# Optimization experiments

Measured on AMD Instinct MI355X. Metric: run time of the kernel, lower is better.

Reference implementation:

```python
import jax, jax.numpy as jnp
import numpy as np

N = 10000; E = 320000; NFEAT = 500; NHID = 256; C = 16; K = 64
GAMMA = 4; ALPHA = 0.1; BETA = 1.0; EPS = 0.1; LAMDA = 0.5; W1 = 0.5

def _init(key, shape, scale=0.05):
    return jax.random.normal(key, shape, dtype=jnp.float32) * scale

def setup_inputs():
    key = jax.random.key(0)
    ks = jax.random.split(key, 24)
    return {
        "x": jax.random.normal(ks[0], (N, NFEAT), dtype=jnp.float32),
        "edge_index": jax.random.randint(ks[1], (2, E), 0, N),
        "edge_weight": jax.random.uniform(ks[2], (E,), dtype=jnp.float32),
        "adj_weight": jax.random.uniform(ks[3], (E,), dtype=jnp.float32),
        "connect": jax.random.uniform(ks[4], (N, N), dtype=jnp.float32),
        "confidence_in": jax.random.uniform(ks[5], (2, E), dtype=jnp.float32),
        "lin1_w": _init(ks[6], (NHID, NFEAT)),
        "lin1_b": jnp.zeros((NHID,), jnp.float32),
        "lin2_w": _init(ks[7], (C, NHID)),
        "lin2_b": jnp.zeros((C,), jnp.float32),
        "lin_a_w": _init(ks[8], (NHID, N), 0.01),
        "lin_a_b": jnp.zeros((NHID,), jnp.float32),
        "lin_n_w": _init(ks[9], (C, C)),
        "lin_n_b": jnp.zeros((C,), jnp.float32),
        "left_w": _init(ks[10], (C, C)),
        "att_w": _init(ks[11], (1, C)),
        "v_w": _init(ks[12], (K, NHID)),
        "v_b": jnp.zeros((K,), jnp.float32),
        "W": _init(ks[13], (C, C)),
        "conf_param": jnp.zeros((3,), jnp.float32),
        "b_param": jnp.zeros((1,), jnp.float32),
    }

def _forward(x, edge_index, edge_weight, adj_weight, connect, confidence_in,
             lin1_w, lin1_b, lin2_w, lin2_b, lin_a_w, lin_a_b, lin_n_w, lin_n_b,
             left_w, att_w, v_w, v_b, W, conf_param, b_param):
    row, col = edge_index[0], edge_index[1]

    def spmm(vals, out_idx, M):
        # COO sparse @ dense: scatter-add per-edge vals * gathered rows of M
        return jax.ops.segment_sum(vals[:, None] * M, out_idx, num_segments=N)

    x_a = connect @ lin_a_w.T + lin_a_b            # [N, NHID]
    h = x @ lin1_w.T + lin1_b
    h = jax.nn.relu((1.0 - LAMDA) * h + LAMDA * x_a)
    raw = h                                        # [N, NHID]
    h = h @ lin2_w.T + lin2_b                      # [N, C]

    # neighbor label distribution: row-normalized adj @ one_hot(argmax softmax)
    y_hat = jnp.argmax(jax.nn.softmax(h, axis=1), axis=1)
    one_hot = jax.nn.one_hot(y_hat, C, dtype=h.dtype)
    nei = spmm(adj_weight, row, one_hot[col])
    s = nei.sum(axis=1, keepdims=True)
    nei = jnp.where(s != 0, nei / jnp.where(s == 0, 1.0, s), 0.0)

    x_n = jax.nn.relu(nei @ lin_n_w.T + lin_n_b)
    h = (1.0 - W1) * h + W1 * x_n
    init = h

    # per-edge attention-based confidence mixed with input confidences
    lx = h @ left_w.T
    confi = jax.nn.relu(lx[row] + lx[col])
    confi = jax.nn.sigmoid((confi @ att_w.T)[:, 0])
    w = jax.nn.softmax(conf_param)
    conf = confi * w[0] + confidence_in[0] * w[1] + confidence_in[1] * w[2]  # [E]

    V = raw @ v_w.T + v_b                          # [N, K]
    U = spmm(adj_weight, row, V[col]) @ jnp.linalg.inv(V.T @ V)
    eyeK = jnp.eye(K, dtype=h.dtype)

    def edge_mask_score(score):
        S = score ** 2
        ss = jnp.sort(S)
        q1, q3 = ss[E // 4], ss[3 * E // 4]
        thr = (q3 + 1.5 * (q3 - q1)) * conf        # [E]
        mask = (S < thr).astype(h.dtype)
        return (score + b_param[0]) * mask

    def update_u(U, V):
        SS = edge_mask_score(edge_weight - jnp.sum(U[row] * V[col], axis=1))
        temp = spmm(SS, row, V[col]) + U @ (V.T @ V) + EPS * (h @ (h.T @ V))
        inver = jnp.linalg.inv((1.0 + EPS) * (V.T @ V) + BETA * eyeK)
        return temp @ inver

    def update_v(U, V):
        SS = edge_mask_score(edge_weight - jnp.sum(V[row] * U[col], axis=1))
        # A^T @ U: scatter over col with U[row]
        temp = spmm(SS, col, U[row]) + V @ (U.T @ U) + EPS * (h @ (h.T @ U))
        inver = jnp.linalg.inv((1.0 + EPS) * (U.T @ U) + BETA * eyeK)
        return temp @ inver

    for j in range(GAMMA):
        if j % 2 == 0:
            U = update_u(U, V)
        else:
            V = update_v(U, V)

    prop = U @ (h.T @ V).T                         # [N, C]
    out = (1.0 - ALPHA) * prop + ALPHA * init
    return out @ W

def reference(x, edge_index, edge_weight, adj_weight, connect, confidence_in,
              lin1_w, lin1_b, lin2_w, lin2_b, lin_a_w, lin_a_b, lin_n_w, lin_n_b,
              left_w, att_w, v_w, v_b, W, conf_param, b_param):
    return _forward(x, edge_index, edge_weight, adj_weight, connect, confidence_in,
                    lin1_w, lin1_b, lin2_w, lin2_b, lin_a_w, lin_a_b, lin_n_w, lin_n_b,
                    left_w, att_w, v_w, v_b, W, conf_param, b_param)
```

## Files before the change

### kernel.cpp

```cpp
#include <hip/hip_runtime.h>
#include <cstddef>
#include <cstdint>


constexpr int kN  = 10000;
constexpr int kE  = 320000;
constexpr int kNH = 256;
constexpr int kC  = 16;
constexpr int kK  = 64;

struct SelState {
  int bin1[2]; int rem1[2];
  float thr_base;
};

typedef short bf16x8 __attribute__((ext_vector_type(8)));
typedef float f32x4 __attribute__((ext_vector_type(4)));
typedef ushort ushort8 __attribute__((ext_vector_type(8)));

__device__ __forceinline__ ushort f2bf(float x) {
  unsigned u = __float_as_uint(x);
  unsigned r = (u + 0x7fffu + ((u >> 16) & 1u)) >> 16;
  return (ushort)r;
}
__device__ __forceinline__ float bf2f(ushort h) {
  return __uint_as_float((unsigned)h << 16);
}
__device__ __forceinline__ int swz(int row, int byteInRow) {
  int chunk = (byteInRow >> 4) ^ ((row >> 1) & 3);
  return row * 64 + (chunk << 4) + (byteInRow & 15);
}

__global__ void split_bf(const float* __restrict__ B, ushort* __restrict__ hi,
                         ushort* __restrict__ lo, int N2, int K, int Kp)
{
  int t = blockIdx.x * 256 + threadIdx.x;
  if (t >= N2 * Kp) return;
  int r = t / Kp, c = t % Kp;
  float v = (c < K) ? B[(size_t)r * K + c] : 0.f;
  ushort h = f2bf(v);
  hi[t] = h;
  lo[t] = f2bf(v - bf2f(h));
}

template<int BN, bool ALO>
__global__ __launch_bounds__(256) void gemm_v3(
    const float* __restrict__ A, const ushort* __restrict__ Bhg,
    const ushort* __restrict__ Blg, const float* __restrict__ bias,
    float* __restrict__ out, int M, int K, int Kp, int KR, int outStride)
{
  __shared__ __align__(16) char sAh[64 * 64];
  __shared__ __align__(16) char sAl[ALO ? 64 * 64 : 16];
  __shared__ __align__(16) char sBh[BN * 64];
  __shared__ __align__(16) char sBl[BN * 64];
  const int t = threadIdx.x;
  const int lane = t & 63, w = t >> 6;
  const int bm = blockIdx.x * 64;
  const int k0 = blockIdx.z * KR;
  const int kend = min(K, k0 + KR);
  out += (size_t)blockIdx.z * M * outStride;
  constexpr int WN = BN / 64;
  constexpr int RB = WN;
  const int wc = (w % WN) * 64;
  const int wr = (w / WN) * (RB * 16);
  const int l15 = lane & 15;
  const int lByte = (lane >> 4) * 16;
  const int ar = t >> 2, ac = t & 3;

  f32x4 acc[RB][4] = {};
  for (int kt = k0; kt < kend; kt += 32) {
    {
      int gr = bm + ar, gk = kt + ac * 8;
      float v[8];
      if (gr < M && gk + 8 <= kend) {
        float4 v0 = *reinterpret_cast<const float4*>(A + (size_t)gr * K + gk);
        float4 v1 = *reinterpret_cast<const float4*>(A + (size_t)gr * K + gk + 4);
        v[0] = v0.x; v[1] = v0.y; v[2] = v0.z; v[3] = v0.w;
        v[4] = v1.x; v[5] = v1.y; v[6] = v1.z; v[7] = v1.w;
      } else {
#pragma unroll
        for (int q = 0; q < 8; q++)
          v[q] = (gr < M && gk + q < kend) ? A[(size_t)gr * K + gk + q] : 0.f;
      }
      ushort8 h8, l8;
#pragma unroll
      for (int q = 0; q < 8; q++) {
        ushort h = f2bf(v[q]); h8[q] = h;
        if (ALO) l8[q] = f2bf(v[q] - bf2f(h));
      }
      *reinterpret_cast<ushort8*>(sAh + swz(ar, ac * 16)) = h8;
      if (ALO) *reinterpret_cast<ushort8*>(sAl + swz(ar, ac * 16)) = l8;
    }
#pragma unroll
    for (int i2 = 0; i2 < BN / 64; i2++) {
      int idx = t + i2 * 256;
      int r = idx >> 2, c = idx & 3;
      size_t gb = (size_t)r * Kp + kt + c * 8;
      ushort8 hv = *reinterpret_cast<const ushort8*>(Bhg + gb);
      ushort8 lv = *reinterpret_cast<const ushort8*>(Blg + gb);
      *reinterpret_cast<ushort8*>(sBh + swz(r, c * 16)) = hv;
      *reinterpret_cast<ushort8*>(sBl + swz(r, c * 16)) = lv;
    }
    __syncthreads();
    bf16x8 bh[4], bl[4];
#pragma unroll
    for (int nb = 0; nb < 4; nb++) {
      int rr = wc + nb * 16 + l15;
      bh[nb] = *reinterpret_cast<const bf16x8*>(sBh + swz(rr, lByte));
      bl[nb] = *reinterpret_cast<const bf16x8*>(sBl + swz(rr, lByte));
    }
#pragma unroll
    for (int rb = 0; rb < RB; rb++) {
      int rr = wr + rb * 16 + l15;
      bf16x8 ah = *reinterpret_cast<const bf16x8*>(sAh + swz(rr, lByte));
#pragma unroll
      for (int nb = 0; nb < 4; nb++) {
        acc[rb][nb] = __builtin_amdgcn_mfma_f32_16x16x32_bf16(ah, bh[nb], acc[rb][nb], 0, 0, 0);
        acc[rb][nb] = __builtin_amdgcn_mfma_f32_16x16x32_bf16(ah, bl[nb], acc[rb][nb], 0, 0, 0);
      }
      if (ALO) {
        bf16x8 al = *reinterpret_cast<const bf16x8*>(sAl + swz(rr, lByte));
#pragma unroll
        for (int nb = 0; nb < 4; nb++)
          acc[rb][nb] = __builtin_amdgcn_mfma_f32_16x16x32_bf16(al, bh[nb], acc[rb][nb], 0, 0, 0);
      }
    }
    __syncthreads();
  }
#pragma unroll
  for (int rb = 0; rb < RB; rb++) {
#pragma unroll
    for (int nb = 0; nb < 4; nb++) {
      int colg = wc + nb * 16 + l15;
      float bv = bias ? bias[colg] : 0.f;
#pragma unroll
      for (int j = 0; j < 4; j++) {
        int rowg = bm + wr + rb * 16 + (lane >> 4) * 4 + j;
        if (rowg < M) out[(size_t)rowg * outStride + colg] = acc[rb][nb][j] + bv;
      }
    }
  }
}

__global__ void reduce_raw(const float4* __restrict__ Pa, const float4* px,
                           const float* __restrict__ ba, const float* __restrict__ b1,
                           float4* rawOut)
{
  int t = blockIdx.x * 256 + threadIdx.x;
  if (t >= kN * kNH / 4) return;
  const int sl = kN * kNH / 4;
  float4 s = Pa[t];
#pragma unroll
  for (int p = 1; p < 6; p++) {
    float4 q = Pa[t + (size_t)p * sl];
    s.x += q.x; s.y += q.y; s.z += q.z; s.w += q.w;
  }
  float4 pxv = px[t];
  int c4 = t & 63;
  float4 vba = reinterpret_cast<const float4*>(ba)[c4];
  float4 vb1 = reinterpret_cast<const float4*>(b1)[c4];
  float4 r;
  r.x = fmaxf(0.5f * (s.x + vba.x) + 0.5f * (pxv.x + vb1.x), 0.f);
  r.y = fmaxf(0.5f * (s.y + vba.y) + 0.5f * (pxv.y + vb1.y), 0.f);
  r.z = fmaxf(0.5f * (s.z + vba.z) + 0.5f * (pxv.z + vb1.z), 0.f);
  r.w = fmaxf(0.5f * (s.w + vba.w) + 0.5f * (pxv.w + vb1.w), 0.f);
  rawOut[t] = r;
}

__global__ void h16_argmax(const float* __restrict__ raw, const float* __restrict__ w2,
                           const float* __restrict__ b2, float* __restrict__ h16,
                           int* __restrict__ yhat, int n)
{
  int t = blockIdx.x * 256 + threadIdx.x;
  if (t >= n * 16) return;
  int i = t >> 4, j = t & 15;
  const float4* a = reinterpret_cast<const float4*>(raw + (size_t)i * 256);
  const float4* b = reinterpret_cast<const float4*>(w2 + (size_t)j * 256);
  float s = b2[j];
#pragma unroll 8
  for (int q = 0; q < 64; q++) {
    float4 av = a[q], bv = b[q];
    s += av.x * bv.x + av.y * bv.y + av.z * bv.z + av.w * bv.w;
  }
  h16[t] = s;
  float m = s; int am = j;
#pragma unroll
  for (int off = 1; off < 16; off <<= 1) {
    float om = __shfl_xor(m, off);
    int oa = __shfl_xor(am, off);
    if (om > m || (om == m && oa < am)) { m = om; am = oa; }
  }
  if (j == 0) yhat[i] = am;
}

__global__ void scatter_nei(const int* __restrict__ row, const int* __restrict__ col,
                            const float* __restrict__ aw, const int* __restrict__ yhat,
                            float* nei, int E)
{
  int e = blockIdx.x * 256 + threadIdx.x;
  if (e >= E) return;
  atomicAdd(&nei[(size_t)row[e] * 16 + yhat[col[e]]], aw[e]);
}

__global__ void norm_xn_h(const float* __restrict__ nei, const float* __restrict__ h16,
                          const float* __restrict__ lnw, const float* __restrict__ lnb,
                          float* __restrict__ hc, int n)
{
  int i = blockIdx.x * 256 + threadIdx.x;
  if (i >= n) return;
  float nv[16]; float s = 0.f;
#pragma unroll
  for (int c = 0; c < 16; c++) { nv[c] = nei[(size_t)i * 16 + c]; s += nv[c]; }
  float inv = (s != 0.f) ? 1.f / s : 0.f;
#pragma unroll
  for (int j = 0; j < 16; j++) {
    float xn = lnb[j];
#pragma unroll
    for (int c = 0; c < 16; c++) xn += (nv[c] * inv) * lnw[j * 16 + c];
    xn = fmaxf(xn, 0.f);
    hc[(size_t)i * 16 + j] = 0.5f * h16[(size_t)i * 16 + j] + 0.5f * xn;
  }
}

__global__ void gemm_rowdot(const float* __restrict__ A, const float* __restrict__ Bw,
                            const float* __restrict__ bias, float* __restrict__ outm,
                            int M, int N2, int K2)
{
  int t = blockIdx.x * 256 + threadIdx.x;
  if (t >= M * N2) return;
  int i = t / N2, j = t % N2;
  const float4* a = reinterpret_cast<const float4*>(A + (size_t)i * K2);
  const float4* b = reinterpret_cast<const float4*>(Bw + (size_t)j * K2);
  float s = bias ? bias[j] : 0.f;
  int q4 = K2 >> 2;
  for (int q = 0; q < q4; q++) {
    float4 av = a[q], bv = b[q];
    s += av.x * bv.x + av.y * bv.y + av.z * bv.z + av.w * bv.w;
  }
  outm[t] = s;
}

__global__ void edge_conf(const int* __restrict__ row, const int* __restrict__ col,
                          const float* __restrict__ lx, const float* __restrict__ attw,
                          const float* __restrict__ ci, const float* __restrict__ cp,
                          float* __restrict__ conf, int E)
{
  int e = blockIdx.x * 256 + threadIdx.x;
  if (e >= E) return;
  float p0 = cp[0], p1 = cp[1], p2 = cp[2];
  float m = fmaxf(p0, fmaxf(p1, p2));
  float e0 = expf(p0 - m), e1 = expf(p1 - m), e2 = expf(p2 - m);
  float inv = 1.f / (e0 + e1 + e2);
  float w0 = e0 * inv, w1 = e1 * inv, w2 = e2 * inv;
  const float* a = lx + (size_t)row[e] * 16;
  const float* b = lx + (size_t)col[e] * 16;
  float s = 0.f;
#pragma unroll
  for (int c = 0; c < 16; c++) s += fmaxf(a[c] + b[c], 0.f) * attw[c];
  float cf = 1.f / (1.f + expf(-s));
  conf[e] = cf * w0 + ci[e] * w1 + ci[(size_t)E + e] * w2;
}

__global__ void csr_count(const int* __restrict__ row, const int* __restrict__ col,
                          int* cntR, int* cntC, int E)
{
  int e = blockIdx.x * 256 + threadIdx.x;
  if (e >= E) return;
  atomicAdd(&cntR[row[e]], 1);
  atomicAdd(&cntC[col[e]], 1);
}

__global__ __launch_bounds__(1024) void scan2(const int* __restrict__ cntR, const int* __restrict__ cntC,
                                              int* __restrict__ startR, int* __restrict__ startC, int n)
{
  __shared__ int part[1024];
  const int t = threadIdx.x;
  for (int pass = 0; pass < 2; ++pass) {
    const int* cnt = pass ? cntC : cntR;
    int* start = pass ? startC : startR;
    int base = t * 10;
    int loc[10]; int s = 0;
#pragma unroll
    for (int q = 0; q < 10; q++) { int idx = base + q; int v = (idx < n) ? cnt[idx] : 0; loc[q] = v; s += v; }
    part[t] = s;
    __syncthreads();
    for (int off = 1; off < 1024; off <<= 1) {
      int v = part[t];
      int u = (t >= off) ? part[t - off] : 0;
      __syncthreads();
      part[t] = v + u;
      __syncthreads();
    }
    int run = part[t] - s;
#pragma unroll
    for (int q = 0; q < 10; q++) { int idx = base + q; if (idx < n) start[idx] = run; run += loc[q]; }
    if (t == 1023) start[n] = part[1023];
    __syncthreads();
  }
}

__global__ void csr_fill(const int* __restrict__ row, const int* __restrict__ col,
                         const int* __restrict__ startR, const int* __restrict__ startC,
                         int* fillR, int* fillC, int* eR, int* eC,
                         int* othR, int* othC, int E)
{
  int e = blockIdx.x * 256 + threadIdx.x;
  if (e >= E) return;
  int r = row[e], c = col[e];
  int pr = startR[r] + atomicAdd(&fillR[r], 1);
  eR[pr] = e; othR[pr] = c;
  int pc = startC[c] + atomicAdd(&fillC[c], 1);
  eC[pc] = e; othC[pc] = r;
}

__global__ void spmm_gather(const float* __restrict__ vals, const float* __restrict__ score,
                            const float* __restrict__ conf, const SelState* __restrict__ sel,
                            const float* __restrict__ bp, const int* __restrict__ start,
                            const int* __restrict__ eids, const int* __restrict__ oth,
                            const float* __restrict__ Msrc, float* __restrict__ T, int n)
{
  int wid = blockIdx.x * 4 + (threadIdx.x >> 6);
  int lane = threadIdx.x & 63;
  if (wid >= n) return;
  float tb = 0.f, bp0 = 0.f;
  if (!vals) { tb = sel->thr_base; bp0 = bp[0]; }
  auto val = [&](int e) -> float {
    if (vals) return vals[e];
    float sc = score[e];
    return (sc * sc < tb * conf[e]) ? (sc + bp0) : 0.f;
  };
  int p = start[wid], pend = start[wid + 1];
  float acc = 0.f;
  for (; p + 4 <= pend; p += 4) {
    int e0 = eids[p], e1 = eids[p + 1], e2 = eids[p + 2], e3 = eids[p + 3];
    int o0 = oth[p], o1 = oth[p + 1], o2 = oth[p + 2], o3 = oth[p + 3];
    float m0 = Msrc[(size_t)o0 * 64 + lane];
    float m1 = Msrc[(size_t)o1 * 64 + lane];
    float m2 = Msrc[(size_t)o2 * 64 + lane];
    float m3 = Msrc[(size_t)o3 * 64 + lane];
    acc += val(e0) * m0 + val(e1) * m1 + val(e2) * m2 + val(e3) * m3;
  }
  for (; p < pend; ++p)
    acc += val(eids[p]) * Msrc[(size_t)oth[p] * 64 + lane];
  T[(size_t)wid * 64 + lane] = acc;
}

__global__ __launch_bounds__(256) void gram2_partial(
    const float* __restrict__ Moth, const float* __restrict__ hc,
    float* __restrict__ P, int n, int chunk)
{
  __shared__ float sM[8 * 64];
  __shared__ float sH[8 * 16];
  const int t = threadIdx.x;
  const int aG = t >> 2, cG0 = (t & 3) * 16;
  const int aH = t >> 4, cH0 = (t & 15) * 4;
  float accG[16];
  float accH[4];
#pragma unroll
  for (int j = 0; j < 16; j++) accG[j] = 0.f;
#pragma unroll
  for (int j = 0; j < 4; j++) accH[j] = 0.f;
  int r0 = blockIdx.x * chunk;
  int r1 = min(n, r0 + chunk);
  for (int rb = r0; rb < r1; rb += 8) {
    int nb = min(8, r1 - rb);
    for (int q = t; q < nb * 64; q += 256) sM[q] = Moth[(size_t)rb * 64 + q];
    for (int q = t; q < nb * 16; q += 256) sH[q] = hc[(size_t)rb * 16 + q];
    __syncthreads();
    for (int r = 0; r < nb; r++) {
      float avG = sM[r * 64 + aG];
      const float* sbG = &sM[r * 64 + cG0];
#pragma unroll
      for (int j = 0; j < 16; j++) accG[j] += avG * sbG[j];
      float avH = sH[r * 16 + aH];
      const float* sbH = &sM[r * 64 + cH0];
#pragma unroll
      for (int j = 0; j < 4; j++) accH[j] += avH * sbH[j];
    }
    __syncthreads();
  }
  float* p1 = P + (size_t)blockIdx.x * 5120 + aG * 64 + cG0;
#pragma unroll
  for (int j = 0; j < 16; j++) p1[j] = accG[j];
  float* p2 = P + (size_t)blockIdx.x * 5120 + 4096 + aH * 64 + cH0;
#pragma unroll
  for (int j = 0; j < 4; j++) p2[j] = accH[j];
}

__global__ void gram_reduce2(const float* __restrict__ P, float* __restrict__ G,
                             float* __restrict__ hTX, int parts)
{
  int c = blockIdx.x * 256 + threadIdx.x;
  if (c >= 5120) return;
  float s = 0.f;
  for (int p = 0; p < parts; p++) s += P[(size_t)p * 5120 + c];
  if (c < 4096) G[c] = s;
  else hTX[c - 4096] = s;
}

__global__ __launch_bounds__(256) void inverse64_spd(
    const float* __restrict__ G, float* __restrict__ Gi, float alpha, float beta,
    const float* __restrict__ hTX, float* __restrict__ Gp, float* __restrict__ Hp)
{
  __shared__ __align__(16) float A[64 * 132];
  __shared__ __align__(16) float prow[128];
  __shared__ float fcol[64];
  const int t = threadIdx.x;
  for (int q = t; q < 64 * 128; q += 256) {
    int r = q >> 7, c = q & 127;
    float v;
    if (c < 64) v = alpha * G[r * 64 + c] + ((c == r) ? beta : 0.f);
    else        v = (c - 64 == r) ? 1.f : 0.f;
    A[r * 132 + c] = v;
  }
  __syncthreads();
  const int i  = t >> 2;
  const int c0 = (t & 3) * 32;
  for (int k = 0; k < 64; k++) {
    if (t < 128) prow[t] = A[k * 132 + t];
    else if (t < 192) fcol[t - 128] = A[(t - 128) * 132 + k];
    __syncthreads();
    float pinv = 1.f / prow[k];
    float f = fcol[i];
    float4* Ar = reinterpret_cast<float4*>(&A[i * 132 + c0]);
    const float4* pr = reinterpret_cast<const float4*>(&prow[c0]);
    if (i == k) {
#pragma unroll
      for (int j = 0; j < 8; j++) {
        float4 p = pr[j];
        p.x *= pinv; p.y *= pinv; p.z *= pinv; p.w *= pinv;
        Ar[j] = p;
      }
    } else {
#pragma unroll
      for (int j = 0; j < 8; j++) {
        float4 p = pr[j]; float4 av = Ar[j];
        av.x -= f * (p.x * pinv); av.y -= f * (p.y * pinv);
        av.z -= f * (p.z * pinv); av.w -= f * (p.w * pinv);
        Ar[j] = av;
      }
    }
    __syncthreads();
  }
  for (int q = t; q < 4096; q += 256) Gi[q] = A[(q >> 6) * 132 + 64 + (q & 63)];
  if (Gp) {
    for (int q = t; q < 4096; q += 256) {
      int r = q >> 6, k = q & 63;
      float s = 0.f;
#pragma unroll 8
      for (int j = 0; j < 64; j++) s += G[r * 64 + j] * A[j * 132 + 64 + k];
      Gp[q] = s;
    }
    for (int q = t; q < 1024; q += 256) {
      int c = q >> 6, k = q & 63;
      float s = 0.f;
#pragma unroll 8
      for (int j = 0; j < 64; j++) s += hTX[c * 64 + j] * A[j * 132 + 64 + k];
      Hp[q] = 0.1f * s;
    }
  }
}

__global__ void edge_score(const float* __restrict__ ew, const int* __restrict__ row,
                           const int* __restrict__ col, const float* __restrict__ Ma,
                           const float* __restrict__ Mb, float* __restrict__ score,
                           int* __restrict__ hist1, int E)
{
  int e = blockIdx.x * 256 + threadIdx.x;
  if (e >= E) return;
  const float4* a = reinterpret_cast<const float4*>(Ma + (size_t)row[e] * 64);
  const float4* b = reinterpret_cast<const float4*>(Mb + (size_t)col[e] * 64);
  float s = 0.f;
#pragma unroll
  for (int q = 0; q < 16; q++) {
    float4 av = a[q], bv = b[q];
    s += av.x * bv.x + av.y * bv.y + av.z * bv.z + av.w * bv.w;
  }
  float sc = ew[e] - s;
  score[e] = sc;
  unsigned u = __float_as_uint(sc * sc);
  atomicAdd(&hist1[u >> 16], 1);
}

__global__ void hist_pass2(const float* __restrict__ score, const SelState* __restrict__ sel,
                           int* __restrict__ h2a, int* __restrict__ h2b, int E)
{
  int e = blockIdx.x * 256 + threadIdx.x;
  if (e >= E) return;
  float sc = score[e];
  unsigned u = __float_as_uint(sc * sc);
  int top = (int)(u >> 16);
  if (top == sel->bin1[0]) atomicAdd(&h2a[u & 0xFFFF], 1);
  if (top == sel->bin1[1]) atomicAdd(&h2b[u & 0xFFFF], 1);
}

__global__ __launch_bounds__(1024) void select_scan(
    const int* __restrict__ h0, const int* __restrict__ h1,
    int stage, SelState* sel)
{
  const int t = threadIdx.x;
  __shared__ int part[1024];
  __shared__ int foundBin[2];
  __shared__ float qsh[2];
  const int per = 64;
  for (int tgt = 0; tgt < 2; tgt++) {
    const int* H = tgt ? h1 : h0;
    const int4* H4 = reinterpret_cast<const int4*>(H + t * per);
    int R = (stage == 1) ? (tgt ? (3 * kE / 4) : (kE / 4)) : sel->rem1[tgt];
    int lsum = 0;
#pragma unroll
    for (int b = 0; b < 16; b++) {
      int4 v = H4[b];
      lsum += v.x + v.y + v.z + v.w;
    }
    part[t] = lsum;
    __syncthreads();
    for (int off = 1; off < 1024; off <<= 1) {
      int v = part[t];
      int u = (t >= off) ? part[t - off] : 0;
      __syncthreads();
      part[t] = v + u;
      __syncthreads();
    }
    int cum = part[t] - lsum;
    int fb = -1, fr = 0;
#pragma unroll
    for (int b = 0; b < 16; b++) {
      int4 v = H4[b];
      int c0 = v.x, c1 = v.y, c2 = v.z, c3 = v.w;
      int bb = t * per + b * 4;
      if (R >= cum && R < cum + c0) { fb = bb; fr = R - cum; }
      cum += c0;
      if (fb < 0 && R >= cum && R < cum + c1) { fb = bb + 1; fr = R - cum; }
      cum += c1;
      if (fb < 0 && R >= cum && R < cum + c2) { fb = bb + 2; fr = R - cum; }
      cum += c2;
      if (fb < 0 && R >= cum && R < cum + c3) { fb = bb + 3; fr = R - cum; }
      cum += c3;
    }
    if (fb >= 0) {
      foundBin[tgt] = fb;
      if (stage == 1) { sel->bin1[tgt] = fb; sel->rem1[tgt] = fr; }
    }
    __syncthreads();
    if (stage == 2 && t == 0) {
      unsigned u = ((unsigned)sel->bin1[tgt] << 16) | (unsigned)foundBin[tgt];
      qsh[tgt] = __uint_as_float(u);
    }
    __syncthreads();
  }
  if (stage == 2 && t == 0) {
    float q1 = qsh[0], q3 = qsh[1];
    sel->thr_base = q3 + 1.5f * (q3 - q1);
  }
}

__global__ void out_fused(const float* __restrict__ T, const float* __restrict__ Gi,
                          const float* __restrict__ X, const float* __restrict__ Gp,
                          const float* __restrict__ hc, const float* __restrict__ Hp,
                          float* __restrict__ Out, int n,
                          int* __restrict__ hist1, int* __restrict__ h2a,
                          int* __restrict__ h2b)
{
  int t = blockIdx.x * 256 + threadIdx.x;
  if (t < 65536) { hist1[t] = 0; h2a[t] = 0; h2b[t] = 0; }
  if (t >= n * 16) return;
  int i = t >> 4, kq = t & 15;
  const float* ti = T + (size_t)i * 64;
  const float4* G4 = reinterpret_cast<const float4*>(Gi);
  float4 s = make_float4(0.f, 0.f, 0.f, 0.f);
#pragma unroll 8
  for (int j = 0; j < 64; j++) {
    float tv = ti[j];
    float4 g = G4[j * 16 + kq];
    s.x += tv * g.x; s.y += tv * g.y; s.z += tv * g.z; s.w += tv * g.w;
  }
  if (X) {
    const float* xi = X + (size_t)i * 64;
    const float4* Gp4 = reinterpret_cast<const float4*>(Gp);
    float4 s2 = make_float4(0.f, 0.f, 0.f, 0.f);
#pragma unroll 8
    for (int j = 0; j < 64; j++) {
      float xv = xi[j];
      float4 g = Gp4[j * 16 + kq];
      s2.x += xv * g.x; s2.y += xv * g.y; s2.z += xv * g.z; s2.w += xv * g.w;
    }
    s.x += s2.x; s.y += s2.y; s.z += s2.z; s.w += s2.w;
    const float4* Hp4 = reinterpret_cast<const float4*>(Hp);
    float4 s3 = make_float4(0.f, 0.f, 0.f, 0.f);
#pragma unroll
    for (int c = 0; c < 16; c++) {
      float hv = hc[(size_t)i * 16 + c];
      float4 g = Hp4[c * 16 + kq];
      s3.x += hv * g.x; s3.y += hv * g.y; s3.z += hv * g.z; s3.w += hv * g.w;
    }
    s.x += s3.x; s.y += s3.y; s.z += s3.z; s.w += s3.w;
  }
  *reinterpret_cast<float4*>(Out + (size_t)i * 64 + kq * 4) = s;
}

__global__ __launch_bounds__(256) void final_out(
    const float* __restrict__ Um, const float* __restrict__ hTV,
    const float* __restrict__ hc, const float* __restrict__ Wm,
    float* __restrict__ out, int n)
{
  __shared__ float sh[1024];
  __shared__ float sW[256];
  for (int q = threadIdx.x; q < 1024; q += 256) sh[q] = hTV[q];
  sW[threadIdx.x] = Wm[threadIdx.x & 255];
  __syncthreads();
  int i = blockIdx.x * 256 + threadIdx.x;
  if (i >= n) return;
  const float* u = Um + (size_t)i * 64;
  float pre[16];
#pragma unroll
  for (int c = 0; c < 16; c++) {
    float s = 0.f;
#pragma unroll
    for (int k = 0; k < 64; k++) s += u[k] * sh[c * 64 + k];
    pre[c] = 0.9f * s + 0.1f * hc[(size_t)i * 16 + c];
  }
#pragma unroll
  for (int j = 0; j < 16; j++) {
    float o = 0.f;
#pragma unroll
    for (int c = 0; c < 16; c++) o += pre[c] * sW[c * 16 + j];
    out[(size_t)i * 16 + j] = o;
  }
}

extern "C" void kernel_launch(void* const* d_in, const int* in_sizes, int n_in,
                              void* d_out, int out_size, void* d_ws, size_t ws_size,
                              hipStream_t stream)
{
  const float* x       = (const float*)d_in[0];
  const int*   eidx    = (const int*)d_in[1];
  const float* ew      = (const float*)d_in[2];
  const float* aw      = (const float*)d_in[3];
  const float* connect = (const float*)d_in[4];
  const float* ci      = (const float*)d_in[5];
  const float* lin1_w  = (const float*)d_in[6];
  const float* lin1_b  = (const float*)d_in[7];
  const float* lin2_w  = (const float*)d_in[8];
  const float* lin2_b  = (const float*)d_in[9];
  const float* lin_a_w = (const float*)d_in[10];
  const float* lin_a_b = (const float*)d_in[11];
  const float* lin_n_w = (const float*)d_in[12];
  const float* lin_n_b = (const float*)d_in[13];
  const float* left_w  = (const float*)d_in[14];
  const float* att_w   = (const float*)d_in[15];
  const float* v_w     = (const float*)d_in[16];
  const float* v_b     = (const float*)d_in[17];
  const float* Wm      = (const float*)d_in[18];
  const float* conf_p  = (const float*)d_in[19];
  const float* b_param = (const float*)d_in[20];
  const int* row = eidx;
  const int* col = eidx + kE;
  float* out = (float*)d_out;

  char* base = (char*)d_ws;
  size_t off = 0;
  auto alloc = [&](size_t bytes) -> void* {
    void* p = base + off;
    off += bytes;
    off = (off + 255) & ~(size_t)255;
    return p;
  };
  float* raw   = (float*)alloc((size_t)kN * kNH * 4);
  float* h16   = (float*)alloc((size_t)kN * kC * 4);
  float* hC    = (float*)alloc((size_t)kN * kC * 4);
  float* nei   = (float*)alloc((size_t)kN * kC * 4);
  float* lx    = (float*)alloc((size_t)kN * kC * 4);
  int*   yhat  = (int*)alloc((size_t)kN * 4);
  float* conf  = (float*)alloc((size_t)kE * 4);
  float* Va    = (float*)alloc((size_t)kN * kK * 4);
  float* Vb    = (float*)alloc((size_t)kN * kK * 4);
  float* Ua    = (float*)alloc((size_t)kN * kK * 4);
  float* Ub    = (float*)alloc((size_t)kN * kK * 4);
  float* T     = (float*)alloc((size_t)kN * kK * 4);
  float* score = (float*)alloc((size_t)kE * 4);
  float* G     = (float*)alloc(64 * 64 * 4);
  float* Gi    = (float*)alloc(64 * 64 * 4);
  float* Gp    = (float*)alloc(64 * 64 * 4);
  float* hTX   = (float*)alloc(kC * kK * 4);
  float* Hp    = (float*)alloc(kC * kK * 4);
  int* hist1   = (int*)alloc(65536 * 4);
  int* h2a     = (int*)alloc(65536 * 4);
  int* h2b     = (int*)alloc(65536 * 4);
  SelState* sel = (SelState*)alloc(sizeof(SelState));
  int* cntR    = (int*)alloc((size_t)kN * 4);
  int* cntC    = (int*)alloc((size_t)kN * 4);
  int* fillR   = (int*)alloc((size_t)kN * 4);
  int* fillC   = (int*)alloc((size_t)kN * 4);
  int* startR  = (int*)alloc((size_t)(kN + 1) * 4);
  int* startC  = (int*)alloc((size_t)(kN + 1) * 4);
  int* eR      = (int*)alloc((size_t)kE * 4);
  int* eC      = (int*)alloc((size_t)kE * 4);
  int* othR    = (int*)alloc((size_t)kE * 4);
  int* othC    = (int*)alloc((size_t)kE * 4);
  float* P     = (float*)alloc((size_t)100 * 5120 * 4);
  const int KpC = 10016, KpX = 512, KpV = 256;
  ushort* BcH = (ushort*)alloc((size_t)256 * KpC * 2);
  ushort* BcL = (ushort*)alloc((size_t)256 * KpC * 2);
  ushort* BxH = (ushort*)alloc((size_t)256 * KpX * 2);
  ushort* BxL = (ushort*)alloc((size_t)256 * KpX * 2);
  ushort* BvH = (ushort*)alloc((size_t)64 * KpV * 2);
  ushort* BvL = (ushort*)alloc((size_t)64 * KpV * 2);
  float* Pbig  = (float*)alloc((size_t)6 * kN * kNH * 4);

  const int eg  = (kE + 255) / 256;
  const int ofg = (kN * 16 + 255) / 256;
  const int gwg = (kN + 3) / 4;

  split_bf<<<(256 * KpC + 255) / 256, 256, 0, stream>>>(lin_a_w, BcH, BcL, 256, 10000, KpC);
  split_bf<<<(256 * KpX + 255) / 256, 256, 0, stream>>>(lin1_w, BxH, BxL, 256, 500, KpX);
  split_bf<<<(64 * KpV + 255) / 256, 256, 0, stream>>>(v_w, BvH, BvL, 64, 256, KpV);

  {
    size_t csrSpan = (size_t)((char*)(fillC + kN) - (char*)cntR);
    (void)hipMemsetAsync(cntR, 0, csrSpan, stream);
  }
  csr_count<<<eg, 256, 0, stream>>>(row, col, cntR, cntC, kE);
  scan2<<<1, 1024, 0, stream>>>(cntR, cntC, startR, startC, kN);
  csr_fill<<<eg, 256, 0, stream>>>(row, col, startR, startC, fillR, fillC, eR, eC, othR, othC, kE);

  gemm_v3<256, false><<<dim3(157, 1, 6), 256, 0, stream>>>(
      connect, BcH, BcL, nullptr, Pbig, kN, 10000, KpC, 1696, kNH);
  gemm_v3<256, true><<<dim3(157, 1, 1), 256, 0, stream>>>(
      x, BxH, BxL, nullptr, raw, kN, 500, KpX, 512, kNH);
  reduce_raw<<<(kN * kNH / 4 + 255) / 256, 256, 0, stream>>>(
      (const float4*)Pbig, (const float4*)raw, lin_a_b, lin1_b, (float4*)raw);
  h16_argmax<<<(kN * 16 + 255) / 256, 256, 0, stream>>>(raw, lin2_w, lin2_b, h16, yhat, kN);
  (void)hipMemsetAsync(nei, 0, (size_t)kN * kC * 4, stream);
  scatter_nei<<<eg, 256, 0, stream>>>(row, col, aw, yhat, nei, kE);
  norm_xn_h<<<(kN + 255) / 256, 256, 0, stream>>>(nei, h16, lin_n_w, lin_n_b, hC, kN);
  gemm_rowdot<<<(kN * kC + 255) / 256, 256, 0, stream>>>(hC, left_w, nullptr, lx, kN, kC, kC);
  edge_conf<<<eg, 256, 0, stream>>>(row, col, lx, att_w, ci, conf_p, conf, kE);
  gemm_v3<64, true><<<dim3(157, 1, 1), 256, 0, stream>>>(
      raw, BvH, BvL, v_b, Va, kN, 256, KpV, 256, kK);

  float* Ucur = Ua; float* Unxt = Ub;
  float* Vcur = Va; float* Vnxt = Vb;

  gram2_partial<<<100, 256, 0, stream>>>(Vcur, hC, P, kN, 100);
  gram_reduce2<<<20, 256, 0, stream>>>(P, G, hTX, 100);
  inverse64_spd<<<1, 256, 0, stream>>>(G, Gi, 1.0f, 0.0f, nullptr, nullptr, nullptr);
  spmm_gather<<<gwg, 256, 0, stream>>>(aw, nullptr, nullptr, nullptr, nullptr,
                                       startR, eR, othR, Vcur, T, kN);
  out_fused<<<ofg, 256, 0, stream>>>(T, Gi, nullptr, nullptr, nullptr, nullptr,
                                     Ucur, kN, hist1, h2a, h2b);

  for (int j = 0; j < 4; j++) {
    bool upd_u = ((j & 1) == 0);
    const float* Ma = upd_u ? Ucur : Vcur;
    const float* Mb = upd_u ? Vcur : Ucur;
    edge_score<<<eg, 256, 0, stream>>>(ew, row, col, Ma, Mb, score, hist1, kE);
    select_scan<<<1, 1024, 0, stream>>>(hist1, hist1, 1, sel);
    hist_pass2<<<eg, 256, 0, stream>>>(score, sel, h2a, h2b, kE);
    select_scan<<<1, 1024, 0, stream>>>(h2a, h2b, 2, sel);

    const float* Xcur = upd_u ? Ucur : Vcur;
    const float* Moth = upd_u ? Vcur : Ucur;
    float* Xout = upd_u ? Unxt : Vnxt;
    gram2_partial<<<100, 256, 0, stream>>>(Moth, hC, P, kN, 100);
    gram_reduce2<<<20, 256, 0, stream>>>(P, G, hTX, 100);
    inverse64_spd<<<1, 256, 0, stream>>>(G, Gi, 1.1f, 1.0f, hTX, Gp, Hp);
    if (upd_u) spmm_gather<<<gwg, 256, 0, stream>>>(nullptr, score, conf, sel, b_param,
                                                    startR, eR, othR, Vcur, T, kN);
    else       spmm_gather<<<gwg, 256, 0, stream>>>(nullptr, score, conf, sel, b_param,
                                                    startC, eC, othC, Ucur, T, kN);
    out_fused<<<ofg, 256, 0, stream>>>(T, Gi, Xcur, Gp, hC, Hp, Xout, kN, hist1, h2a, h2b);
    if (upd_u) { float* tmp = Ucur; Ucur = Unxt; Unxt = tmp; }
    else       { float* tmp = Vcur; Vcur = Vnxt; Vnxt = tmp; }
  }

  gram2_partial<<<100, 256, 0, stream>>>(Vcur, hC, P, kN, 100);
  gram_reduce2<<<20, 256, 0, stream>>>(P, G, hTX, 100);
  final_out<<<(kN + 255) / 256, 256, 0, stream>>>(Ucur, hTX, hC, Wm, out, kN);
}
```

Before: 2.220 ms.

## Fuse post-GEMM pipeline into a persistent cooperative megakernel with grid syncs

Replaces the long chain of small kernel launches (CSR build, neighbor label scatter, edge confidence, gram partials, inverse, edge scoring, histogram selection, SpMM, output) with one cooperative persistent kernel. Phases are separated by grid-wide syncs, and independent small work such as the scan and the 64x64 inverse is placed on different blocks within the same phase. The gram partial count also changes. The aim is to remove per-launch overhead and idle gaps between many tiny dependent kernels. In exchange, each phase is limited to the resident grid size and pays grid-sync latency, and a fallback of per-phase launches covers the case where the cooperative launch fails.

Result: slower. 5.853 ms (+163.7%).

```diff
diff --git a/kernel.cpp b/kernel.cpp
--- a/kernel.cpp
+++ b/kernel.cpp
@@ -1,6 +1,9 @@
 #include <hip/hip_runtime.h>
+#include <hip/hip_cooperative_groups.h>
 #include <cstddef>
 #include <cstdint>
+
+namespace cg = cooperative_groups;
 
 
 constexpr int kN  = 10000;
@@ -8,6 +11,7 @@
 constexpr int kNH = 256;
 constexpr int kC  = 16;
 constexpr int kK  = 64;
+constexpr int GRAM_PARTS = 256;
 
 struct SelState {
   int bin1[2]; int rem1[2];
@@ -104,25 +108,25 @@
     __syncthreads();
     bf16x8 bh[4], bl[4];
 #pragma unroll
-    for (int nb = 0; nb < 4; nb++) {
-      int rr = wc + nb * 16 + l15;
-      bh[nb] = *reinterpret_cast<const bf16x8*>(sBh + swz(rr, lByte));
-      bl[nb] = *reinterpret_cast<const bf16x8*>(sBl + swz(rr, lByte));
+    for (int nbq = 0; nbq < 4; nbq++) {
+      int rr = wc + nbq * 16 + l15;
+      bh[nbq] = *reinterpret_cast<const bf16x8*>(sBh + swz(rr, lByte));
+      bl[nbq] = *reinterpret_cast<const bf16x8*>(sBl + swz(rr, lByte));
     }
 #pragma unroll
     for (int rb = 0; rb < RB; rb++) {
       int rr = wr + rb * 16 + l15;
       bf16x8 ah = *reinterpret_cast<const bf16x8*>(sAh + swz(rr, lByte));
 #pragma unroll
-      for (int nb = 0; nb < 4; nb++) {
-        acc[rb][nb] = __builtin_amdgcn_mfma_f32_16x16x32_bf16(ah, bh[nb], acc[rb][nb], 0, 0, 0);
-        acc[rb][nb] = __builtin_amdgcn_mfma_f32_16x16x32_bf16(ah, bl[nb], acc[rb][nb], 0, 0, 0);
+      for (int nbq = 0; nbq < 4; nbq++) {
+        acc[rb][nbq] = __builtin_amdgcn_mfma_f32_16x16x32_bf16(ah, bh[nbq], acc[rb][nbq], 0, 0, 0);
+        acc[rb][nbq] = __builtin_amdgcn_mfma_f32_16x16x32_bf16(ah, bl[nbq], acc[rb][nbq], 0, 0, 0);
       }
       if (ALO) {
         bf16x8 al = *reinterpret_cast<const bf16x8*>(sAl + swz(rr, lByte));
 #pragma unroll
-        for (int nb = 0; nb < 4; nb++)
-          acc[rb][nb] = __builtin_amdgcn_mfma_f32_16x16x32_bf16(al, bh[nb], acc[rb][nb], 0, 0, 0);
+        for (int nbq = 0; nbq < 4; nbq++)
+          acc[rb][nbq] = __builtin_amdgcn_mfma_f32_16x16x32_bf16(al, bh[nbq], acc[rb][nbq], 0, 0, 0);
       }
     }
     __syncthreads();
@@ -130,13 +134,13 @@
 #pragma unroll
   for (int rb = 0; rb < RB; rb++) {
 #pragma unroll
-    for (int nb = 0; nb < 4; nb++) {
-      int colg = wc + nb * 16 + l15;
+    for (int nbq = 0; nbq < 4; nbq++) {
+      int colg = wc + nbq * 16 + l15;
       float bv = bias ? bias[colg] : 0.f;
 #pragma unroll
-      for (int j = 0; j < 4; j++) {
-        int rowg = bm + wr + rb * 16 + (lane >> 4) * 4 + j;
-        if (rowg < M) out[(size_t)rowg * outStride + colg] = acc[rb][nb][j] + bv;
+      for (int jj = 0; jj < 4; jj++) {
+        int rowg = bm + wr + rb * 16 + (lane >> 4) * 4 + jj;
+        if (rowg < M) out[(size_t)rowg * outStride + colg] = acc[rb][nbq][jj] + bv;
       }
     }
   }
@@ -167,244 +171,80 @@
   rawOut[t] = r;
 }
 
-__global__ void h16_argmax(const float* __restrict__ raw, const float* __restrict__ w2,
-                           const float* __restrict__ b2, float* __restrict__ h16,
-                           int* __restrict__ yhat, int n)
-{
-  int t = blockIdx.x * 256 + threadIdx.x;
-  if (t >= n * 16) return;
-  int i = t >> 4, j = t & 15;
-  const float4* a = reinterpret_cast<const float4*>(raw + (size_t)i * 256);
-  const float4* b = reinterpret_cast<const float4*>(w2 + (size_t)j * 256);
-  float s = b2[j];
-#pragma unroll 8
-  for (int q = 0; q < 64; q++) {
-    float4 av = a[q], bv = b[q];
-    s += av.x * bv.x + av.y * bv.y + av.z * bv.z + av.w * bv.w;
-  }
-  h16[t] = s;
-  float m = s; int am = j;
-#pragma unroll
-  for (int off = 1; off < 16; off <<= 1) {
-    float om = __shfl_xor(m, off);
-    int oa = __shfl_xor(am, off);
-    if (om > m || (om == m && oa < am)) { m = om; am = oa; }
-  }
-  if (j == 0) yhat[i] = am;
-}
-
-__global__ void scatter_nei(const int* __restrict__ row, const int* __restrict__ col,
-                            const float* __restrict__ aw, const int* __restrict__ yhat,
-                            float* nei, int E)
-{
-  int e = blockIdx.x * 256 + threadIdx.x;
-  if (e >= E) return;
-  atomicAdd(&nei[(size_t)row[e] * 16 + yhat[col[e]]], aw[e]);
-}
-
-__global__ void norm_xn_h(const float* __restrict__ nei, const float* __restrict__ h16,
-                          const float* __restrict__ lnw, const float* __restrict__ lnb,
-                          float* __restrict__ hc, int n)
-{
-  int i = blockIdx.x * 256 + threadIdx.x;
-  if (i >= n) return;
-  float nv[16]; float s = 0.f;
-#pragma unroll
-  for (int c = 0; c < 16; c++) { nv[c] = nei[(size_t)i * 16 + c]; s += nv[c]; }
-  float inv = (s != 0.f) ? 1.f / s : 0.f;
-#pragma unroll
-  for (int j = 0; j < 16; j++) {
-    float xn = lnb[j];
-#pragma unroll
-    for (int c = 0; c < 16; c++) xn += (nv[c] * inv) * lnw[j * 16 + c];
-    xn = fmaxf(xn, 0.f);
-    hc[(size_t)i * 16 + j] = 0.5f * h16[(size_t)i * 16 + j] + 0.5f * xn;
-  }
-}
-
-__global__ void gemm_rowdot(const float* __restrict__ A, const float* __restrict__ Bw,
-                            const float* __restrict__ bias, float* __restrict__ outm,
-                            int M, int N2, int K2)
-{
-  int t = blockIdx.x * 256 + threadIdx.x;
-  if (t >= M * N2) return;
-  int i = t / N2, j = t % N2;
-  const float4* a = reinterpret_cast<const float4*>(A + (size_t)i * K2);
-  const float4* b = reinterpret_cast<const float4*>(Bw + (size_t)j * K2);
-  float s = bias ? bias[j] : 0.f;
-  int q4 = K2 >> 2;
-  for (int q = 0; q < q4; q++) {
-    float4 av = a[q], bv = b[q];
-    s += av.x * bv.x + av.y * bv.y + av.z * bv.z + av.w * bv.w;
-  }
-  outm[t] = s;
-}
-
-__global__ void edge_conf(const int* __restrict__ row, const int* __restrict__ col,
-                          const float* __restrict__ lx, const float* __restrict__ attw,
-                          const float* __restrict__ ci, const float* __restrict__ cp,
-                          float* __restrict__ conf, int E)
-{
-  int e = blockIdx.x * 256 + threadIdx.x;
-  if (e >= E) return;
-  float p0 = cp[0], p1 = cp[1], p2 = cp[2];
-  float m = fmaxf(p0, fmaxf(p1, p2));
-  float e0 = expf(p0 - m), e1 = expf(p1 - m), e2 = expf(p2 - m);
-  float inv = 1.f / (e0 + e1 + e2);
-  float w0 = e0 * inv, w1 = e1 * inv, w2 = e2 * inv;
-  const float* a = lx + (size_t)row[e] * 16;
-  const float* b = lx + (size_t)col[e] * 16;
-  float s = 0.f;
-#pragma unroll
-  for (int c = 0; c < 16; c++) s += fmaxf(a[c] + b[c], 0.f) * attw[c];
-  float cf = 1.f / (1.f + expf(-s));
-  conf[e] = cf * w0 + ci[e] * w1 + ci[(size_t)E + e] * w2;
-}
-
-__global__ void csr_count(const int* __restrict__ row, const int* __restrict__ col,
-                          int* cntR, int* cntC, int E)
-{
-  int e = blockIdx.x * 256 + threadIdx.x;
-  if (e >= E) return;
-  atomicAdd(&cntR[row[e]], 1);
-  atomicAdd(&cntC[col[e]], 1);
-}
-
-__global__ __launch_bounds__(1024) void scan2(const int* __restrict__ cntR, const int* __restrict__ cntC,
-                                              int* __restrict__ startR, int* __restrict__ startC, int n)
-{
-  __shared__ int part[1024];
-  const int t = threadIdx.x;
-  for (int pass = 0; pass < 2; ++pass) {
-    const int* cnt = pass ? cntC : cntR;
-    int* start = pass ? startC : startR;
-    int base = t * 10;
-    int loc[10]; int s = 0;
-#pragma unroll
-    for (int q = 0; q < 10; q++) { int idx = base + q; int v = (idx < n) ? cnt[idx] : 0; loc[q] = v; s += v; }
-    part[t] = s;
-    __syncthreads();
-    for (int off = 1; off < 1024; off <<= 1) {
-      int v = part[t];
-      int u = (t >= off) ? part[t - off] : 0;
-      __syncthreads();
-      part[t] = v + u;
-      __syncthreads();
-    }
-    int run = part[t] - s;
-#pragma unroll
-    for (int q = 0; q < 10; q++) { int idx = base + q; if (idx < n) start[idx] = run; run += loc[q]; }
-    if (t == 1023) start[n] = part[1023];
-    __syncthreads();
-  }
-}
-
-__global__ void csr_fill(const int* __restrict__ row, const int* __restrict__ col,
-                         const int* __restrict__ startR, const int* __restrict__ startC,
-                         int* fillR, int* fillC, int* eR, int* eC,
-                         int* othR, int* othC, int E)
-{
-  int e = blockIdx.x * 256 + threadIdx.x;
-  if (e >= E) return;
-  int r = row[e], c = col[e];
-  int pr = startR[r] + atomicAdd(&fillR[r], 1);
-  eR[pr] = e; othR[pr] = c;
-  int pc = startC[c] + atomicAdd(&fillC[c], 1);
-  eC[pc] = e; othC[pc] = r;
-}
-
-__global__ void spmm_gather(const float* __restrict__ vals, const float* __restrict__ score,
-                            const float* __restrict__ conf, const SelState* __restrict__ sel,
-                            const float* __restrict__ bp, const int* __restrict__ start,
-                            const int* __restrict__ eids, const int* __restrict__ oth,
-                            const float* __restrict__ Msrc, float* __restrict__ T, int n)
-{
-  int wid = blockIdx.x * 4 + (threadIdx.x >> 6);
-  int lane = threadIdx.x & 63;
-  if (wid >= n) return;
-  float tb = 0.f, bp0 = 0.f;
-  if (!vals) { tb = sel->thr_base; bp0 = bp[0]; }
-  auto val = [&](int e) -> float {
-    if (vals) return vals[e];
-    float sc = score[e];
-    return (sc * sc < tb * conf[e]) ? (sc + bp0) : 0.f;
-  };
-  int p = start[wid], pend = start[wid + 1];
-  float acc = 0.f;
-  for (; p + 4 <= pend; p += 4) {
-    int e0 = eids[p], e1 = eids[p + 1], e2 = eids[p + 2], e3 = eids[p + 3];
-    int o0 = oth[p], o1 = oth[p + 1], o2 = oth[p + 2], o3 = oth[p + 3];
-    float m0 = Msrc[(size_t)o0 * 64 + lane];
-    float m1 = Msrc[(size_t)o1 * 64 + lane];
-    float m2 = Msrc[(size_t)o2 * 64 + lane];
-    float m3 = Msrc[(size_t)o3 * 64 + lane];
-    acc += val(e0) * m0 + val(e1) * m1 + val(e2) * m2 + val(e3) * m3;
-  }
-  for (; p < pend; ++p)
-    acc += val(eids[p]) * Msrc[(size_t)oth[p] * 64 + lane];
-  T[(size_t)wid * 64 + lane] = acc;
-}
-
-__global__ __launch_bounds__(256) void gram2_partial(
-    const float* __restrict__ Moth, const float* __restrict__ hc,
-    float* __restrict__ P, int n, int chunk)
-{
-  __shared__ float sM[8 * 64];
-  __shared__ float sH[8 * 16];
+struct MegaArgs {
+  const float* raw;
+  const float* lin2_w; const float* lin2_b;
+  const int* row; const int* col;
+  const float* aw; const float* ew;
+  const float* lnw; const float* lnb;
+  const float* left_w; const float* att_w;
+  const float* ci; const float* conf_p; const float* b_param;
+  const float* Wm;
+  float* h16; int* yhat; float* nei; float* hC; float* lx; float* conf;
+  int* cntR; int* cntC; int* fillR; int* fillC; int* startR; int* startC;
+  int* eR; int* eC; int* othR; int* othC;
+  float* Va; float* Vb; float* Ua; float* Ub; float* T;
+  float* score; float* G; float* Gi; float* Gp; float* hTX; float* Hp;
+  int* hist1; int* h2a; int* h2b;
+  float* P;
+  SelState* sel;
+  float* out;
+};
+
+__device__ __forceinline__ void uv_at(const MegaArgs& a, int j,
+                                      float*& Ucur, float*& Unxt,
+                                      float*& Vcur, float*& Vnxt)
+{
+  int uU = (j >= 1) + (j >= 3);
+  int uV = (j >= 2) + (j >= 4);
+  Ucur = (uU & 1) ? a.Ub : a.Ua; Unxt = (uU & 1) ? a.Ua : a.Ub;
+  Vcur = (uV & 1) ? a.Vb : a.Va; Vnxt = (uV & 1) ? a.Va : a.Vb;
+}
+
+__device__ void gram2_dev(const float* M, const float* hc, float* P, int b, float* shm)
+{
+  float* sM = shm;
+  float* sH = shm + 512;
   const int t = threadIdx.x;
   const int aG = t >> 2, cG0 = (t & 3) * 16;
   const int aH = t >> 4, cH0 = (t & 15) * 4;
-  float accG[16];
-  float accH[4];
-#pragma unroll
-  for (int j = 0; j < 16; j++) accG[j] = 0.f;
-#pragma unroll
-  for (int j = 0; j < 4; j++) accH[j] = 0.f;
-  int r0 = blockIdx.x * chunk;
-  int r1 = min(n, r0 + chunk);
+  float accG[16]; float accH[4];
+#pragma unroll
+  for (int q = 0; q < 16; q++) accG[q] = 0.f;
+#pragma unroll
+  for (int q = 0; q < 4; q++) accH[q] = 0.f;
+  int r0 = b * 40, r1 = min(kN, r0 + 40);
   for (int rb = r0; rb < r1; rb += 8) {
-    int nb = min(8, r1 - rb);
-    for (int q = t; q < nb * 64; q += 256) sM[q] = Moth[(size_t)rb * 64 + q];
-    for (int q = t; q < nb * 16; q += 256) sH[q] = hc[(size_t)rb * 16 + q];
-    __syncthreads();
-    for (int r = 0; r < nb; r++) {
+    int nb2 = min(8, r1 - rb);
+    __syncthreads();
+    for (int q = t; q < nb2 * 64; q += 256) sM[q] = M[(size_t)rb * 64 + q];
+    for (int q = t; q < nb2 * 16; q += 256) sH[q] = hc[(size_t)rb * 16 + q];
+    __syncthreads();
+    for (int r = 0; r < nb2; r++) {
       float avG = sM[r * 64 + aG];
       const float* sbG = &sM[r * 64 + cG0];
 #pragma unroll
-      for (int j = 0; j < 16; j++) accG[j] += avG * sbG[j];
+      for (int q = 0; q < 16; q++) accG[q] += avG * sbG[q];
       float avH = sH[r * 16 + aH];
       const float* sbH = &sM[r * 64 + cH0];
 #pragma unroll
-      for (int j = 0; j < 4; j++) accH[j] += avH * sbH[j];
-    }
-    __syncthreads();
-  }
-  float* p1 = P + (size_t)blockIdx.x * 5120 + aG * 64 + cG0;
-#pragma unroll
-  for (int j = 0; j < 16; j++) p1[j] = accG[j];
-  float* p2 = P + (size_t)blockIdx.x * 5120 + 4096 + aH * 64 + cH0;
-#pragma unroll
-  for (int j = 0; j < 4; j++) p2[j] = accH[j];
-}
-
-__global__ void gram_reduce2(const float* __restrict__ P, float* __restrict__ G,
-                             float* __restrict__ hTX, int parts)
-{
-  int c = blockIdx.x * 256 + threadIdx.x;
-  if (c >= 5120) return;
-  float s = 0.f;
-  for (int p = 0; p < parts; p++) s += P[(size_t)p * 5120 + c];
-  if (c < 4096) G[c] = s;
-  else hTX[c - 4096] = s;
-}
-
-__global__ __launch_bounds__(256) void inverse64_spd(
-    const float* __restrict__ G, float* __restrict__ Gi, float alpha, float beta,
-    const float* __restrict__ hTX, float* __restrict__ Gp, float* __restrict__ Hp)
-{
-  __shared__ __align__(16) float A[64 * 132];
-  __shared__ __align__(16) float prow[128];
-  __shared__ float fcol[64];
+      for (int q = 0; q < 4; q++) accH[q] += avH * sbH[q];
+    }
+  }
+  float* p1 = P + (size_t)b * 5120 + aG * 64 + cG0;
+#pragma unroll
+  for (int q = 0; q < 16; q++) p1[q] = accG[q];
+  float* p2 = P + (size_t)b * 5120 + 4096 + aH * 64 + cH0;
+#pragma unroll
+  for (int q = 0; q < 4; q++) p2[q] = accH[q];
+}
+
+__device__ void inverse_dev(const float* G, float* Gi, float alpha, float beta,
+                            const float* hTX, float* Gp, float* Hp, float* shm)
+{
+  float* A = shm;
+  float* prow = shm + 8448;
+  float* fcol = shm + 8576;
   const int t = threadIdx.x;
   for (int q = t; q < 64 * 128; q += 256) {
     int r = q >> 7, c = q & 127;
@@ -426,18 +266,18 @@
     const float4* pr = reinterpret_cast<const float4*>(&prow[c0]);
     if (i == k) {
 #pragma unroll
-      for (int j = 0; j < 8; j++) {
-        float4 p = pr[j];
+      for (int q = 0; q < 8; q++) {
+        float4 p = pr[q];
         p.x *= pinv; p.y *= pinv; p.z *= pinv; p.w *= pinv;
-        Ar[j] = p;
+        Ar[q] = p;
       }
     } else {
 #pragma unroll
-      for (int j = 0; j < 8; j++) {
-        float4 p = pr[j]; float4 av = Ar[j];
+      for (int q = 0; q < 8; q++) {
+        float4 p = pr[q]; float4 av = Ar[q];
         av.x -= f * (p.x * pinv); av.y -= f * (p.y * pinv);
         av.z -= f * (p.z * pinv); av.w -= f * (p.w * pinv);
-        Ar[j] = av;
+        Ar[q] = av;
       }
     }
     __syncthreads();
@@ -448,74 +288,34 @@
       int r = q >> 6, k = q & 63;
       float s = 0.f;
 #pragma unroll 8
-      for (int j = 0; j < 64; j++) s += G[r * 64 + j] * A[j * 132 + 64 + k];
+      for (int jj = 0; jj < 64; jj++) s += G[r * 64 + jj] * A[jj * 132 + 64 + k];
       Gp[q] = s;
     }
     for (int q = t; q < 1024; q += 256) {
       int c = q >> 6, k = q & 63;
       float s = 0.f;
 #pragma unroll 8
-      for (int j = 0; j < 64; j++) s += hTX[c * 64 + j] * A[j * 132 + 64 + k];
+      for (int jj = 0; jj < 64; jj++) s += hTX[c * 64 + jj] * A[jj * 132 + 64 + k];
       Hp[q] = 0.1f * s;
     }
   }
 }
 
-__global__ void edge_score(const float* __restrict__ ew, const int* __restrict__ row,
-                           const int* __restrict__ col, const float* __restrict__ Ma,
-                           const float* __restrict__ Mb, float* __restrict__ score,
-                           int* __restrict__ hist1, int E)
-{
-  int e = blockIdx.x * 256 + threadIdx.x;
-  if (e >= E) return;
-  const float4* a = reinterpret_cast<const float4*>(Ma + (size_t)row[e] * 64);
-  const float4* b = reinterpret_cast<const float4*>(Mb + (size_t)col[e] * 64);
-  float s = 0.f;
-#pragma unroll
-  for (int q = 0; q < 16; q++) {
-    float4 av = a[q], bv = b[q];
-    s += av.x * bv.x + av.y * bv.y + av.z * bv.z + av.w * bv.w;
-  }
-  float sc = ew[e] - s;
-  score[e] = sc;
-  unsigned u = __float_as_uint(sc * sc);
-  atomicAdd(&hist1[u >> 16], 1);
-}
-
-__global__ void hist_pass2(const float* __restrict__ score, const SelState* __restrict__ sel,
-                           int* __restrict__ h2a, int* __restrict__ h2b, int E)
-{
-  int e = blockIdx.x * 256 + threadIdx.x;
-  if (e >= E) return;
-  float sc = score[e];
-  unsigned u = __float_as_uint(sc * sc);
-  int top = (int)(u >> 16);
-  if (top == sel->bin1[0]) atomicAdd(&h2a[u & 0xFFFF], 1);
-  if (top == sel->bin1[1]) atomicAdd(&h2b[u & 0xFFFF], 1);
-}
-
-__global__ __launch_bounds__(1024) void select_scan(
-    const int* __restrict__ h0, const int* __restrict__ h1,
-    int stage, SelState* sel)
+__device__ void scan_dev(const int* h0, const int* h1, int stage, SelState* sel, int* shm)
 {
   const int t = threadIdx.x;
-  __shared__ int part[1024];
-  __shared__ int foundBin[2];
-  __shared__ float qsh[2];
-  const int per = 64;
+  int* part = shm;
+  int* fbs  = shm + 256;
+  float* qsh = (float*)(shm + 258);
   for (int tgt = 0; tgt < 2; tgt++) {
     const int* H = tgt ? h1 : h0;
-    const int4* H4 = reinterpret_cast<const int4*>(H + t * per);
+    const int4* H4 = reinterpret_cast<const int4*>(H + t * 256);
     int R = (stage == 1) ? (tgt ? (3 * kE / 4) : (kE / 4)) : sel->rem1[tgt];
     int lsum = 0;
-#pragma unroll
-    for (int b = 0; b < 16; b++) {
-      int4 v = H4[b];
-      lsum += v.x + v.y + v.z + v.w;
-    }
+    for (int b = 0; b < 64; b++) { int4 v = H4[b]; lsum += v.x + v.y + v.z + v.w; }
     part[t] = lsum;
     __syncthreads();
-    for (int off = 1; off < 1024; off <<= 1) {
+    for (int off = 1; off < 256; off <<= 1) {
       int v = part[t];
       int u = (t >= off) ? part[t - off] : 0;
       __syncthreads();
@@ -524,27 +324,21 @@
     }
     int cum = part[t] - lsum;
     int fb = -1, fr = 0;
-#pragma unroll
-    for (int b = 0; b < 16; b++) {
+    for (int b = 0; b < 64; b++) {
       int4 v = H4[b];
-      int c0 = v.x, c1 = v.y, c2 = v.z, c3 = v.w;
-      int bb = t * per + b * 4;
-      if (R >= cum && R < cum + c0) { fb = bb; fr = R - cum; }
-      cum += c0;
-      if (fb < 0 && R >= cum && R < cum + c1) { fb = bb + 1; fr = R - cum; }
-      cum += c1;
-      if (fb < 0 && R >= cum && R < cum + c2) { fb = bb + 2; fr = R - cum; }
-      cum += c2;
-      if (fb < 0 && R >= cum && R < cum + c3) { fb = bb + 3; fr = R - cum; }
-      cum += c3;
+      int bb = t * 256 + b * 4;
+      if (fb < 0 && R >= cum && R < cum + v.x) { fb = bb;     fr = R - cum; } cum += v.x;
+      if (fb < 0 && R >= cum && R < cum + v.y) { fb = bb + 1; fr = R - cum; } cum += v.y;
+      if (fb < 0 && R >= cum && R < cum + v.z) { fb = bb + 2; fr = R - cum; } cum += v.z;
+      if (fb < 0 && R >= cum && R < cum + v.w) { fb = bb + 3; fr = R - cum; } cum += v.w;
     }
     if (fb >= 0) {
-      foundBin[tgt] = fb;
+      fbs[tgt] = fb;
       if (stage == 1) { sel->bin1[tgt] = fb; sel->rem1[tgt] = fr; }
     }
     __syncthreads();
     if (stage == 2 && t == 0) {
-      unsigned u = ((unsigned)sel->bin1[tgt] << 16) | (unsigned)foundBin[tgt];
+      unsigned u = ((unsigned)sel->bin1[tgt] << 16) | (unsigned)fbs[tgt];
       qsh[tgt] = __uint_as_float(u);
     }
     __syncthreads();
@@ -555,78 +349,331 @@
   }
 }
 
-__global__ void out_fused(const float* __restrict__ T, const float* __restrict__ Gi,
-                          const float* __restrict__ X, const float* __restrict__ Gp,
-                          const float* __restrict__ hc, const float* __restrict__ Hp,
-                          float* __restrict__ Out, int n,
-                          int* __restrict__ hist1, int* __restrict__ h2a,
-                          int* __restrict__ h2b)
-{
-  int t = blockIdx.x * 256 + threadIdx.x;
-  if (t < 65536) { hist1[t] = 0; h2a[t] = 0; h2b[t] = 0; }
-  if (t >= n * 16) return;
-  int i = t >> 4, kq = t & 15;
-  const float* ti = T + (size_t)i * 64;
-  const float4* G4 = reinterpret_cast<const float4*>(Gi);
-  float4 s = make_float4(0.f, 0.f, 0.f, 0.f);
+__device__ void spmm_dev(const float* vals, const float* score, const float* conf,
+                         const SelState* sel, const float* bp,
+                         const int* start, const int* eids, const int* oth,
+                         const float* Msrc, float* T, int wid0, int wstride)
+{
+  int lane = threadIdx.x & 63;
+  float tb = 0.f, bp0 = 0.f;
+  if (!vals) { tb = sel->thr_base; bp0 = bp[0]; }
+  for (int wid = wid0; wid < kN; wid += wstride) {
+    int p = start[wid], pend = start[wid + 1];
+    float acc = 0.f;
+    for (; p + 4 <= pend; p += 4) {
+      int e0 = eids[p], e1 = eids[p + 1], e2 = eids[p + 2], e3 = eids[p + 3];
+      int o0 = oth[p], o1 = oth[p + 1], o2 = oth[p + 2], o3 = oth[p + 3];
+      float m0 = Msrc[(size_t)o0 * 64 + lane];
+      float m1 = Msrc[(size_t)o1 * 64 + lane];
+      float m2 = Msrc[(size_t)o2 * 64 + lane];
+      float m3 = Msrc[(size_t)o3 * 64 + lane];
+      float v0, v1, v2, v3;
+      if (vals) { v0 = vals[e0]; v1 = vals[e1]; v2 = vals[e2]; v3 = vals[e3]; }
+      else {
+        float s0 = score[e0], s1 = score[e1], s2 = score[e2], s3 = score[e3];
+        v0 = (s0 * s0 < tb * conf[e0]) ? (s0 + bp0) : 0.f;
+        v1 = (s1 * s1 < tb * conf[e1]) ? (s1 + bp0) : 0.f;
+        v2 = (s2 * s2 < tb * conf[e2]) ? (s2 + bp0) : 0.f;
+        v3 = (s3 * s3 < tb * conf[e3]) ? (s3 + bp0) : 0.f;
+      }
+      acc += v0 * m0 + v1 * m1 + v2 * m2 + v3 * m3;
+    }
+    for (; p < pend; ++p) {
+      int e = eids[p];
+      float v;
+      if (vals) v = vals[e];
+      else { float sc = score[e]; v = (sc * sc < tb * conf[e]) ? (sc + bp0) : 0.f; }
+      acc += v * Msrc[(size_t)oth[p] * 64 + lane];
+    }
+    T[(size_t)wid * 64 + lane] = acc;
+  }
+}
+
+__device__ void outf_dev(const MegaArgs& a, const float* T, const float* X,
+                         float* Out, int gtid, int gsz)
+{
+  for (int i = gtid; i < 65536; i += gsz) { a.hist1[i] = 0; a.h2a[i] = 0; a.h2b[i] = 0; }
+  for (int t = gtid; t < kN * 16; t += gsz) {
+    int i = t >> 4, kq = t & 15;
+    const float* ti = T + (size_t)i * 64;
+    const float4* G4 = reinterpret_cast<const float4*>(a.Gi);
+    float4 s = make_float4(0.f, 0.f, 0.f, 0.f);
 #pragma unroll 8
-  for (int j = 0; j < 64; j++) {
-    float tv = ti[j];
-    float4 g = G4[j * 16 + kq];
-    s.x += tv * g.x; s.y += tv * g.y; s.z += tv * g.z; s.w += tv * g.w;
-  }
-  if (X) {
-    const float* xi = X + (size_t)i * 64;
-    const float4* Gp4 = reinterpret_cast<const float4*>(Gp);
-    float4 s2 = make_float4(0.f, 0.f, 0.f, 0.f);
+    for (int jj = 0; jj < 64; jj++) {
+      float tv = ti[jj];
+      float4 g = G4[jj * 16 + kq];
+      s.x += tv * g.x; s.y += tv * g.y; s.z += tv * g.z; s.w += tv * g.w;
+    }
+    if (X) {
+      const float* xi = X + (size_t)i * 64;
+      const float4* Gp4 = reinterpret_cast<const float4*>(a.Gp);
+      float4 s2 = make_float4(0.f, 0.f, 0.f, 0.f);
 #pragma unroll 8
-    for (int j = 0; j < 64; j++) {
-      float xv = xi[j];
-      float4 g = Gp4[j * 16 + kq];
-      s2.x += xv * g.x; s2.y += xv * g.y; s2.z += xv * g.z; s2.w += xv * g.w;
-    }
-    s.x += s2.x; s.y += s2.y; s.z += s2.z; s.w += s2.w;
-    const float4* Hp4 = reinterpret_cast<const float4*>(Hp);
-    float4 s3 = make_float4(0.f, 0.f, 0.f, 0.f);
-#pragma unroll
-    for (int c = 0; c < 16; c++) {
-      float hv = hc[(size_t)i * 16 + c];
-      float4 g = Hp4[c * 16 + kq];
-      s3.x += hv * g.x; s3.y += hv * g.y; s3.z += hv * g.z; s3.w += hv * g.w;
-    }
-    s.x += s3.x; s.y += s3.y; s.z += s3.z; s.w += s3.w;
-  }
-  *reinterpret_cast<float4*>(Out + (size_t)i * 64 + kq * 4) = s;
-}
-
-__global__ __launch_bounds__(256) void final_out(
-    const float* __restrict__ Um, const float* __restrict__ hTV,
-    const float* __restrict__ hc, const float* __restrict__ Wm,
-    float* __restrict__ out, int n)
-{
-  __shared__ float sh[1024];
-  __shared__ float sW[256];
-  for (int q = threadIdx.x; q < 1024; q += 256) sh[q] = hTV[q];
-  sW[threadIdx.x] = Wm[threadIdx.x & 255];
-  __syncthreads();
-  int i = blockIdx.x * 256 + threadIdx.x;
-  if (i >= n) return;
-  const float* u = Um + (size_t)i * 64;
-  float pre[16];
-#pragma unroll
-  for (int c = 0; c < 16; c++) {
+      for (int jj = 0; jj < 64; jj++) {
+        float xv = xi[jj];
+        float4 g = Gp4[jj * 16 + kq];
+        s2.x += xv * g.x; s2.y += xv * g.y; s2.z += xv * g.z; s2.w += xv * g.w;
+      }
+      s.x += s2.x; s.y += s2.y; s.z += s2.z; s.w += s2.w;
+      const float4* Hp4 = reinterpret_cast<const float4*>(a.Hp);
+      float4 s3 = make_float4(0.f, 0.f, 0.f, 0.f);
+#pragma unroll
+      for (int c = 0; c < 16; c++) {
+        float hv = a.hC[(size_t)i * 16 + c];
+        float4 g = Hp4[c * 16 + kq];
+        s3.x += hv * g.x; s3.y += hv * g.y; s3.z += hv * g.z; s3.w += hv * g.w;
+      }
+      s.x += s3.x; s.y += s3.y; s.z += s3.z; s.w += s3.w;
+    }
+    *reinterpret_cast<float4*>(Out + (size_t)i * 64 + kq * 4) = s;
+  }
+}
+
+__device__ void reduce_dev(const MegaArgs& a, int gtid, int gsz)
+{
+  for (int c = gtid; c < 5120; c += gsz) {
     float s = 0.f;
-#pragma unroll
-    for (int k = 0; k < 64; k++) s += u[k] * sh[c * 64 + k];
-    pre[c] = 0.9f * s + 0.1f * hc[(size_t)i * 16 + c];
-  }
-#pragma unroll
-  for (int j = 0; j < 16; j++) {
-    float o = 0.f;
-#pragma unroll
-    for (int c = 0; c < 16; c++) o += pre[c] * sW[c * 16 + j];
-    out[(size_t)i * 16 + j] = o;
-  }
+    for (int p = 0; p < GRAM_PARTS; p++) s += a.P[(size_t)p * 5120 + c];
+    if (c < 4096) a.G[c] = s;
+    else a.hTX[c - 4096] = s;
+  }
+}
+
+__device__ void run_phase(const MegaArgs& a, int phase, int j, float* smem)
+{
+  const int tid = threadIdx.x;
+  const int bid = blockIdx.x;
+  const int nb  = gridDim.x;
+  const int gtid = bid * 256 + tid;
+  const int gsz = nb * 256;
+  float *Ucur, *Unxt, *Vcur, *Vnxt;
+  uv_at(a, j, Ucur, Unxt, Vcur, Vnxt);
+  bool up = ((j & 1) == 0);
+  const float* Ma   = up ? Ucur : Vcur;
+  const float* Mb   = up ? Vcur : Ucur;
+  const float* Moth = up ? Vcur : Ucur;
+  const float* Xcur = up ? Ucur : Vcur;
+  float* Xout       = up ? Unxt : Vnxt;
+
+  switch (phase) {
+  case 0: {
+    for (int i = gtid; i < kN; i += gsz) { a.cntR[i] = 0; a.cntC[i] = 0; a.fillR[i] = 0; a.fillC[i] = 0; }
+    for (int t = gtid; t < kN * 16; t += gsz) {
+      int i = t >> 4, jj = t & 15;
+      const float4* av4 = reinterpret_cast<const float4*>(a.raw + (size_t)i * 256);
+      const float4* bv4 = reinterpret_cast<const float4*>(a.lin2_w + (size_t)jj * 256);
+      float s = a.lin2_b[jj];
+#pragma unroll 8
+      for (int q = 0; q < 64; q++) {
+        float4 av = av4[q], bv = bv4[q];
+        s += av.x * bv.x + av.y * bv.y + av.z * bv.z + av.w * bv.w;
+      }
+      a.h16[t] = s;
+      float m = s; int am = jj;
+#pragma unroll
+      for (int off = 1; off < 16; off <<= 1) {
+        float om = __shfl_xor(m, off);
+        int oa = __shfl_xor(am, off);
+        if (om > m || (om == m && oa < am)) { m = om; am = oa; }
+      }
+      if (jj == 0) a.yhat[i] = am;
+      a.nei[t] = 0.f;
+    }
+    for (int i = gtid; i < 65536; i += gsz) { a.hist1[i] = 0; a.h2a[i] = 0; a.h2b[i] = 0; }
+  } break;
+  case 1: {
+    for (int e = gtid; e < kE; e += gsz) {
+      int r = a.row[e], c = a.col[e];
+      atomicAdd(&a.cntR[r], 1);
+      atomicAdd(&a.cntC[c], 1);
+      atomicAdd(&a.nei[(size_t)r * 16 + a.yhat[c]], a.aw[e]);
+    }
+  } break;
+  case 2: {
+    if (bid == 0) {
+      int* part = (int*)smem;
+      for (int pass = 0; pass < 2; ++pass) {
+        const int* cnt = pass ? a.cntC : a.cntR;
+        int* start = pass ? a.startC : a.startR;
+        int bbase = tid * 40;
+        int s = 0;
+        for (int q = 0; q < 40; q++) { int idx = bbase + q; if (idx < kN) s += cnt[idx]; }
+        part[tid] = s;
+        __syncthreads();
+        for (int off = 1; off < 256; off <<= 1) {
+          int v = part[tid];
+          int u = (tid >= off) ? part[tid - off] : 0;
+          __syncthreads();
+          part[tid] = v + u;
+          __syncthreads();
+        }
+        int run = part[tid] - s;
+        for (int q = 0; q < 40; q++) {
+          int idx = bbase + q;
+          if (idx < kN) { start[idx] = run; run += cnt[idx]; }
+        }
+        if (tid == 255) start[kN] = part[255];
+        __syncthreads();
+      }
+    } else {
+      for (int i = (bid - 1) * 256 + tid; i < kN; i += (nb - 1) * 256) {
+        float nv[16]; float s = 0.f;
+#pragma unroll
+        for (int c = 0; c < 16; c++) { nv[c] = a.nei[(size_t)i * 16 + c]; s += nv[c]; }
+        float inv = (s != 0.f) ? 1.f / s : 0.f;
+#pragma unroll
+        for (int jj = 0; jj < 16; jj++) {
+          float xn = a.lnb[jj];
+#pragma unroll
+          for (int c = 0; c < 16; c++) xn += (nv[c] * inv) * a.lnw[jj * 16 + c];
+          xn = fmaxf(xn, 0.f);
+          a.hC[(size_t)i * 16 + jj] = 0.5f * a.h16[(size_t)i * 16 + jj] + 0.5f * xn;
+        }
+      }
+    }
+  } break;
+  case 3: {
+    for (int e = gtid; e < kE; e += gsz) {
+      int r = a.row[e], c = a.col[e];
+      int pr = a.startR[r] + atomicAdd(&a.fillR[r], 1);
+      a.eR[pr] = e; a.othR[pr] = c;
+      int pc = a.startC[c] + atomicAdd(&a.fillC[c], 1);
+      a.eC[pc] = e; a.othC[pc] = r;
+    }
+    for (int t = gtid; t < kN * 16; t += gsz) {
+      int i = t >> 4, jj = t & 15;
+      float s = 0.f;
+#pragma unroll
+      for (int c = 0; c < 16; c++) s += a.hC[(size_t)i * 16 + c] * a.left_w[jj * 16 + c];
+      a.lx[t] = s;
+    }
+  } break;
+  case 4: {
+    for (int e = gtid; e < kE; e += gsz) {
+      float p0 = a.conf_p[0], p1 = a.conf_p[1], p2 = a.conf_p[2];
+      float m = fmaxf(p0, fmaxf(p1, p2));
+      float e0 = expf(p0 - m), e1 = expf(p1 - m), e2 = expf(p2 - m);
+      float inv = 1.f / (e0 + e1 + e2);
+      float w0 = e0 * inv, w1 = e1 * inv, w2 = e2 * inv;
+      const float* aa = a.lx + (size_t)a.row[e] * 16;
+      const float* bb = a.lx + (size_t)a.col[e] * 16;
+      float s = 0.f;
+#pragma unroll
+      for (int c = 0; c < 16; c++) s += fmaxf(aa[c] + bb[c], 0.f) * a.att_w[c];
+      float cf = 1.f / (1.f + expf(-s));
+      a.conf[e] = cf * w0 + a.ci[e] * w1 + a.ci[(size_t)kE + e] * w2;
+    }
+    for (int part = bid; part < GRAM_PARTS; part += nb)
+      gram2_dev(a.Va, a.hC, a.P, part, smem);
+  } break;
+  case 5: reduce_dev(a, gtid, gsz); break;
+  case 6: {
+    if (bid == 0) inverse_dev(a.G, a.Gi, 1.0f, 0.0f, nullptr, nullptr, nullptr, smem);
+    else spmm_dev(a.aw, nullptr, nullptr, nullptr, nullptr,
+                  a.startR, a.eR, a.othR, a.Va, a.T,
+                  (bid - 1) * 4 + (tid >> 6), (nb - 1) * 4);
+  } break;
+  case 7: outf_dev(a, a.T, nullptr, a.Ua, gtid, gsz); break;
+  case 8: {
+    for (int e = gtid; e < kE; e += gsz) {
+      const float4* av4 = reinterpret_cast<const float4*>(Ma + (size_t)a.row[e] * 64);
+      const float4* bv4 = reinterpret_cast<const float4*>(Mb + (size_t)a.col[e] * 64);
+      float s = 0.f;
+#pragma unroll
+      for (int q = 0; q < 16; q++) {
+        float4 av = av4[q], bv = bv4[q];
+        s += av.x * bv.x + av.y * bv.y + av.z * bv.z + av.w * bv.w;
+      }
+      float sc = a.ew[e] - s;
+      a.score[e] = sc;
+      unsigned u = __float_as_uint(sc * sc);
+      atomicAdd(&a.hist1[u >> 16], 1);
+    }
+  } break;
+  case 9: {
+    if (bid == 0) scan_dev(a.hist1, a.hist1, 1, a.sel, (int*)smem);
+    else for (int part = bid - 1; part < GRAM_PARTS; part += nb - 1)
+      gram2_dev(Moth, a.hC, a.P, part, smem);
+  } break;
+  case 10: {
+    reduce_dev(a, gtid, gsz);
+    for (int e = gtid; e < kE; e += gsz) {
+      float sc = a.score[e];
+      unsigned u = __float_as_uint(sc * sc);
+      int top = (int)(u >> 16);
+      if (top == a.sel->bin1[0]) atomicAdd(&a.h2a[u & 0xFFFF], 1);
+      if (top == a.sel->bin1[1]) atomicAdd(&a.h2b[u & 0xFFFF], 1);
+    }
+  } break;
+  case 11: {
+    if (bid == 0) scan_dev(a.h2a, a.h2b, 2, a.sel, (int*)smem);
+    else if (bid == 1) inverse_dev(a.G, a.Gi, 1.1f, 1.0f, a.hTX, a.Gp, a.Hp, smem);
+  } break;
+  case 12: {
+    if (up) spmm_dev(nullptr, a.score, a.conf, a.sel, a.b_param,
+                     a.startR, a.eR, a.othR, Vcur, a.T, bid * 4 + (tid >> 6), nb * 4);
+    else    spmm_dev(nullptr, a.score, a.conf, a.sel, a.b_param,
+                     a.startC, a.eC, a.othC, Ucur, a.T, bid * 4 + (tid >> 6), nb * 4);
+  } break;
+  case 13: outf_dev(a, a.T, Xcur, Xout, gtid, gsz); break;
+  case 14: {
+    for (int part = bid; part < GRAM_PARTS; part += nb)
+      gram2_dev(Vcur, a.hC, a.P, part, smem);
+  } break;
+  case 15: reduce_dev(a, gtid, gsz); break;
+  case 16: {
+    float* sh = smem;
+    float* sW = smem + 1024;
+    for (int q = tid; q < 1024; q += 256) sh[q] = a.hTX[q];
+    sW[tid] = a.Wm[tid & 255];
+    __syncthreads();
+    for (int i = gtid; i < kN; i += gsz) {
+      const float* u = Ucur + (size_t)i * 64;
+      float pre[16];
+#pragma unroll
+      for (int c = 0; c < 16; c++) {
+        float s = 0.f;
+#pragma unroll
+        for (int k = 0; k < 64; k++) s += u[k] * sh[c * 64 + k];
+        pre[c] = 0.9f * s + 0.1f * a.hC[(size_t)i * 16 + c];
+      }
+#pragma unroll
+      for (int jj = 0; jj < 16; jj++) {
+        float o = 0.f;
+#pragma unroll
+        for (int c = 0; c < 16; c++) o += pre[c] * sW[c * 16 + jj];
+        a.out[(size_t)i * 16 + jj] = o;
+      }
+    }
+  } break;
+  }
+}
+
+__global__ __launch_bounds__(256, 4) void mega(MegaArgs a)
+{
+  cg::grid_group grid = cg::this_grid();
+  __shared__ __align__(16) float smem[8704];
+  for (int p = 0; p <= 7; p++) {
+    run_phase(a, p, 0, smem);
+    __threadfence(); grid.sync();
+  }
+  for (int j = 0; j < 4; j++) {
+    for (int p = 8; p <= 13; p++) {
+      run_phase(a, p, j, smem);
+      __threadfence(); grid.sync();
+    }
+  }
+  run_phase(a, 14, 4, smem);
+  __threadfence(); grid.sync();
+  run_phase(a, 15, 4, smem);
+  __threadfence(); grid.sync();
+  run_phase(a, 16, 4, smem);
+}
+
+__global__ __launch_bounds__(256, 4) void mega_phase(MegaArgs a, int phase, int j)
+{
+  __shared__ __align__(16) float smem[8704];
+  run_phase(a, phase, j, smem);
 }
 
 extern "C" void kernel_launch(void* const* d_in, const int* in_sizes, int n_in,
@@ -698,7 +745,7 @@
   int* eC      = (int*)alloc((size_t)kE * 4);
   int* othR    = (int*)alloc((size_t)kE * 4);
   int* othC    = (int*)alloc((size_t)kE * 4);
-  float* P     = (float*)alloc((size_t)100 * 5120 * 4);
+  float* P     = (float*)alloc((size_t)GRAM_PARTS * 5120 * 4);
   const int KpC = 10016, KpX = 512, KpV = 256;
   ushort* BcH = (ushort*)alloc((size_t)256 * KpC * 2);
   ushort* BcL = (ushort*)alloc((size_t)256 * KpC * 2);
@@ -708,21 +755,9 @@
   ushort* BvL = (ushort*)alloc((size_t)64 * KpV * 2);
   float* Pbig  = (float*)alloc((size_t)6 * kN * kNH * 4);
 
-  const int eg  = (kE + 255) / 256;
-  const int ofg = (kN * 16 + 255) / 256;
-  const int gwg = (kN + 3) / 4;
-
   split_bf<<<(256 * KpC + 255) / 256, 256, 0, stream>>>(lin_a_w, BcH, BcL, 256, 10000, KpC);
   split_bf<<<(256 * KpX + 255) / 256, 256, 0, stream>>>(lin1_w, BxH, BxL, 256, 500, KpX);
   split_bf<<<(64 * KpV + 255) / 256, 256, 0, stream>>>(v_w, BvH, BvL, 64, 256, KpV);
-
-  {
-    size_t csrSpan = (size_t)((char*)(fillC + kN) - (char*)cntR);
-    (void)hipMemsetAsync(cntR, 0, csrSpan, stream);
-  }
-  csr_count<<<eg, 256, 0, stream>>>(row, col, cntR, cntC, kE);
-  scan2<<<1, 1024, 0, stream>>>(cntR, cntC, startR, startC, kN);
-  csr_fill<<<eg, 256, 0, stream>>>(row, col, startR, startC, fillR, fillC, eR, eC, othR, othC, kE);
 
   gemm_v3<256, false><<<dim3(157, 1, 6), 256, 0, stream>>>(
       connect, BcH, BcL, nullptr, Pbig, kN, 10000, KpC, 1696, kNH);
@@ -730,51 +765,46 @@
       x, BxH, BxL, nullptr, raw, kN, 500, KpX, 512, kNH);
   reduce_raw<<<(kN * kNH / 4 + 255) / 256, 256, 0, stream>>>(
       (const float4*)Pbig, (const float4*)raw, lin_a_b, lin1_b, (float4*)raw);
-  h16_argmax<<<(kN * 16 + 255) / 256, 256, 0, stream>>>(raw, lin2_w, lin2_b, h16, yhat, kN);
-  (void)hipMemsetAsync(nei, 0, (size_t)kN * kC * 4, stream);
-  scatter_nei<<<eg, 256, 0, stream>>>(row, col, aw, yhat, nei, kE);
-  norm_xn_h<<<(kN + 255) / 256, 256, 0, stream>>>(nei, h16, lin_n_w, lin_n_b, hC, kN);
-  gemm_rowdot<<<(kN * kC + 255) / 256, 256, 0, stream>>>(hC, left_w, nullptr, lx, kN, kC, kC);
-  edge_conf<<<eg, 256, 0, stream>>>(row, col, lx, att_w, ci, conf_p, conf, kE);
   gemm_v3<64, true><<<dim3(157, 1, 1), 256, 0, stream>>>(
       raw, BvH, BvL, v_b, Va, kN, 256, KpV, 256, kK);
 
-  float* Ucur = Ua; float* Unxt = Ub;
-  float* Vcur = Va; float* Vnxt = Vb;
-
-  gram2_partial<<<100, 256, 0, stream>>>(Vcur, hC, P, kN, 100);
-  gram_reduce2<<<20, 256, 0, stream>>>(P, G, hTX, 100);
-  inverse64_spd<<<1, 256, 0, stream>>>(G, Gi, 1.0f, 0.0f, nullptr, nullptr, nullptr);
-  spmm_gather<<<gwg, 256, 0, stream>>>(aw, nullptr, nullptr, nullptr, nullptr,
-                                       startR, eR, othR, Vcur, T, kN);
-  out_fused<<<ofg, 256, 0, stream>>>(T, Gi, nullptr, nullptr, nullptr, nullptr,
-                                     Ucur, kN, hist1, h2a, h2b);
-
-  for (int j = 0; j < 4; j++) {
-    bool upd_u = ((j & 1) == 0);
-    const float* Ma = upd_u ? Ucur : Vcur;
-    const float* Mb = upd_u ? Vcur : Ucur;
-    edge_score<<<eg, 256, 0, stream>>>(ew, row, col, Ma, Mb, score, hist1, kE);
-    select_scan<<<1, 1024, 0, stream>>>(hist1, hist1, 1, sel);
-    hist_pass2<<<eg, 256, 0, stream>>>(score, sel, h2a, h2b, kE);
-    select_scan<<<1, 1024, 0, stream>>>(h2a, h2b, 2, sel);
-
-    const float* Xcur = upd_u ? Ucur : Vcur;
-    const float* Moth = upd_u ? Vcur : Ucur;
-    float* Xout = upd_u ? Unxt : Vnxt;
-    gram2_partial<<<100, 256, 0, stream>>>(Moth, hC, P, kN, 100);
-    gram_reduce2<<<20, 256, 0, stream>>>(P, G, hTX, 100);
-    inverse64_spd<<<1, 256, 0, stream>>>(G, Gi, 1.1f, 1.0f, hTX, Gp, Hp);
-    if (upd_u) spmm_gather<<<gwg, 256, 0, stream>>>(nullptr, score, conf, sel, b_param,
-                                                    startR, eR, othR, Vcur, T, kN);
-    else       spmm_gather<<<gwg, 256, 0, stream>>>(nullptr, score, conf, sel, b_param,
-                                                    startC, eC, othC, Ucur, T, kN);
-    out_fused<<<ofg, 256, 0, stream>>>(T, Gi, Xcur, Gp, hC, Hp, Xout, kN, hist1, h2a, h2b);
-    if (upd_u) { float* tmp = Ucur; Ucur = Unxt; Unxt = tmp; }
-    else       { float* tmp = Vcur; Vcur = Vnxt; Vnxt = tmp; }
-  }
-
-  gram2_partial<<<100, 256, 0, stream>>>(Vcur, hC, P, kN, 100);
-  gram_reduce2<<<20, 256, 0, stream>>>(P, G, hTX, 100);
-  final_out<<<(kN + 255) / 256, 256, 0, stream>>>(Ucur, hTX, hC, Wm, out, kN);
-}
+  MegaArgs ma;
+  ma.raw = raw; ma.lin2_w = lin2_w; ma.lin2_b = lin2_b;
+  ma.row = row; ma.col = col; ma.aw = aw; ma.ew = ew;
+  ma.lnw = lin_n_w; ma.lnb = lin_n_b; ma.left_w = left_w; ma.att_w = att_w;
+  ma.ci = ci; ma.conf_p = conf_p; ma.b_param = b_param; ma.Wm = Wm;
+  ma.h16 = h16; ma.yhat = yhat; ma.nei = nei; ma.hC = hC; ma.lx = lx; ma.conf = conf;
+  ma.cntR = cntR; ma.cntC = cntC; ma.fillR = fillR; ma.fillC = fillC;
+  ma.startR = startR; ma.startC = startC;
+  ma.eR = eR; ma.eC = eC; ma.othR = othR; ma.othC = othC;
+  ma.Va = Va; ma.Vb = Vb; ma.Ua = Ua; ma.Ub = Ub; ma.T = T;
+  ma.score = score; ma.G = G; ma.Gi = Gi; ma.Gp = Gp; ma.hTX = hTX; ma.Hp = Hp;
+  ma.hist1 = hist1; ma.h2a = h2a; ma.h2b = h2b;
+  ma.P = P; ma.sel = sel; ma.out = out;
+
+  int dev = 0;
+  (void)hipGetDevice(&dev);
+  int numCU = 0;
+  (void)hipDeviceGetAttribute(&numCU, hipDeviceAttributeMultiprocessorCount, dev);
+  int maxPerCU = 0;
+  hipError_t oe = hipOccupancyMaxActiveBlocksPerMultiprocessor(
+      &maxPerCU, (const void*)mega, 256, 0);
+  int grid = 768;
+  if (oe == hipSuccess && numCU > 0 && maxPerCU > 0) {
+    long cap = (long)maxPerCU * numCU;
+    if (cap < grid) grid = (int)cap;
+  }
+  if (grid < 2) grid = 2;
+
+  void* args[] = { &ma };
+  hipError_t err = hipLaunchCooperativeKernel((const void*)mega, dim3(grid), dim3(256),
+                                              args, 0, stream);
+  if (err != hipSuccess) {
+    for (int p = 0; p <= 7; p++) mega_phase<<<640, 256, 0, stream>>>(ma, p, 0);
+    for (int j = 0; j < 4; j++)
+      for (int p = 8; p <= 13; p++) mega_phase<<<640, 256, 0, stream>>>(ma, p, j);
+    mega_phase<<<640, 256, 0, stream>>>(ma, 14, 4);
+    mega_phase<<<640, 256, 0, stream>>>(ma, 15, 4);
+    mega_phase<<<640, 256, 0, stream>>>(ma, 16, 4);
+  }
+}
```
